# Performance work log

Hardware: AMD Instinct MI355X
Metric: run time of the kernel (lower is better)

Reference implementation:

```python
import jax, jax.numpy as jnp
import numpy as np

N = 25600   # total nodes
B = 256     # graphs / batch_size / LSTM seq length
F = 128     # num_feat
H = 256     # gnn_hidden
R = 512     # rnn_hidden == 2*H (forced by alm layer)
L = 2       # rnn_layers
V = 32000   # vocab
E = 409600  # edges
NPG = 100   # nodes per graph (forced by alm layer / attention reshape)


def setup_inputs() -> dict:
    key = jax.random.key(0)
    ks = jax.random.split(key, 20)
    def rn(k, shape, fan_in, scale=1.0):
        return jax.random.normal(k, shape, jnp.float32) * (scale / np.sqrt(fan_in))
    inp = {}
    inp['x'] = jax.random.normal(ks[0], (N, F), jnp.float32)
    inp['edge_index'] = jax.random.randint(ks[1], (2, E), 0, N)
    inp['bwd_edge_index'] = jnp.flip(inp['edge_index'], axis=0)
    inp['batch'] = jnp.arange(N) // NPG  # contiguous graphs, 100 nodes each
    inp['h0'] = jax.random.normal(ks[2], (L, 1, R), jnp.float32)
    inp['c0'] = jax.random.normal(ks[3], (L, 1, R), jnp.float32)
    inp['W_gnn'] = rn(ks[4], (F, H), F)
    inp['W_root'] = rn(ks[5], (H, H), H)
    inp['W_nbr'] = rn(ks[6], (H, H), H)
    inp['b_conv'] = jnp.zeros((H,), jnp.float32)
    D = 2 * H
    inp['W1'] = rn(ks[7], (D, D), D); inp['b1'] = jnp.zeros((D,), jnp.float32)
    inp['gamma'] = jnp.ones((D,), jnp.float32); inp['beta'] = jnp.zeros((D,), jnp.float32)
    inp['W2'] = rn(ks[8], (D, D), D); inp['b2'] = jnp.zeros((D,), jnp.float32)
    A = NPG * R + R  # alm input dim = rnn_hidden*100 + rnn_hidden
    inp['W_alm'] = rn(ks[9], (NPG, A), A, scale=0.1)
    inp['b_alm'] = jnp.ones((NPG,), jnp.float32)  # keeps alpha.sum() well away from 0
    inp['Wih0'] = rn(ks[10], (4 * R, D), D); inp['Whh0'] = rn(ks[11], (4 * R, R), R)
    inp['bih0'] = jnp.zeros((4 * R,), jnp.float32); inp['bhh0'] = jnp.zeros((4 * R,), jnp.float32)
    inp['Wih1'] = rn(ks[12], (4 * R, R), R); inp['Whh1'] = rn(ks[13], (4 * R, R), R)
    inp['bih1'] = jnp.zeros((4 * R,), jnp.float32); inp['bhh1'] = jnp.zeros((4 * R,), jnp.float32)
    inp['W_fc'] = rn(ks[14], (R, V), R); inp['b_fc'] = jnp.zeros((V,), jnp.float32)
    return inp


def _lstm_layer(inputs, h, c, Wih, Whh, bih, bhh):
    # inputs: (T, 1, in); carry h, c: (1, R). PyTorch gate order i, f, g, o.
    def step(carry, xt):
        h, c = carry
        g = xt @ Wih.T + bih + h @ Whh.T + bhh
        i, f, gg, o = jnp.split(g, 4, axis=-1)
        c = jax.nn.sigmoid(f) * c + jax.nn.sigmoid(i) * jnp.tanh(gg)
        h = jax.nn.sigmoid(o) * jnp.tanh(c)
        return (h, c), h
    (hT, cT), outs = jax.lax.scan(step, (h, c), inputs)
    return outs, hT, cT


def reference(x, edge_index, bwd_edge_index, batch, h0, c0, W_gnn, W_root, W_nbr, b_conv,
              W1, b1, gamma, beta, W2, b2, W_alm, b_alm,
              Wih0, Whh0, bih0, bhh0, Wih1, Whh1, bih1, bhh1, W_fc, b_fc):
    n = x.shape[0]
    x = x @ W_gnn  # (N, H)
    # GraphConv: out_i = W_root x_i + W_nbr * sum_{j->i} x_j + b.
    # (Original loops gnn_layers times from the SAME x, so only the last conv matters.)
    def conv(xx, ei):
        agg = jax.ops.segment_sum(xx[ei[0]], ei[1], num_segments=n)
        return xx @ W_root + agg @ W_nbr + b_conv
    fwd_x = jax.nn.relu(conv(x, edge_index))
    bwd_x = jax.nn.relu(conv(x, bwd_edge_index))
    xc = jnp.concatenate([fwd_x, bwd_x], axis=1)  # (N, 2H) == (N, R)
    # MLP [2H, 2H, 2H]: Lin -> BatchNorm(batch stats) -> ReLU -> (dropout off) -> Lin
    h1 = xc @ W1 + b1
    h1 = (h1 - h1.mean(0)) / jnp.sqrt(h1.var(0) + 1e-5) * gamma + beta
    x_mlp = jax.nn.relu(h1) @ W2 + b2
    # global mean pool over graphs
    counts = jax.ops.segment_sum(jnp.ones((n,), x_mlp.dtype), batch, num_segments=B)
    x_g = jax.ops.segment_sum(x_mlp, batch, num_segments=B) / counts[:, None]
    x_emb = x_g.reshape(B, 1, 2 * H)  # LSTM: seq_len=B, batch=1
    # attention over cell state (vectorized form of the nested loops):
    # alpha[l,b,:] = alm(cat(c0[l].flatten(), h3[b].flatten())); normalize by sum (NOT softmax);
    # new_c[l] = sum_b alpha[l,b,:] @ h3[b]
    h3 = xc.reshape(B, NPG, R)
    s = c0.reshape(L, R)
    Ws, Wh = W_alm[:, :R], W_alm[:, R:]
    alpha = (s @ Ws.T)[:, None, :] + (h3.reshape(B, NPG * R) @ Wh.T)[None] + b_alm  # (L,B,NPG)
    alpha = alpha / alpha.sum(-1, keepdims=True)
    new_c = jnp.einsum('lbk,bkd->ld', alpha, h3)  # (L, R)
    # 2-layer LSTM (eval mode: inter-layer dropout is identity)
    outs, hT0, cT0 = _lstm_layer(x_emb, h0[0], new_c[0:1], Wih0, Whh0, bih0, bhh0)
    outs, hT1, cT1 = _lstm_layer(outs, h0[1], new_c[1:2], Wih1, Whh1, bih1, bhh1)
    preds = (outs @ W_fc + b_fc)[:, -1, :]  # (B, V)
    return preds
```

## Files before the change

kernel.cpp:

```cpp
#include <hip/hip_runtime.h>
#include <math.h>

#define N_NODES 25600
#define F_IN    128
#define H_GNN   256
#define D_MLP   512
#define E_EDGE  409600
#define B_GR    256
#define NPG_    100
#define R_LSTM  512
#define V_OUT   32000

typedef __bf16 bf16x8 __attribute__((ext_vector_type(8)));
typedef float  f32x4  __attribute__((ext_vector_type(4)));
typedef unsigned short u16x8 __attribute__((ext_vector_type(8)));

__device__ __forceinline__ unsigned short f2bf(float x) {
    unsigned u = __builtin_bit_cast(unsigned, x);
    unsigned r = (u + 0x7FFFu + ((u >> 16) & 1u)) >> 16;
    return (unsigned short)r;
}

template<bool TRANSB>
__global__ __launch_bounds__(256)
void gemm_tile(const float* __restrict__ A, const float* __restrict__ B,
               float* __restrict__ C, const float* __restrict__ bias,
               int M, int N, int K, int lda, int ldb, int ldc, int kChunk)
{
    __shared__ float As[16][68];
    __shared__ float Bs[16][68];
    const int tid = threadIdx.x;
    const int n0 = blockIdx.x * 64;
    const int m0 = blockIdx.y * 64;
    const int z  = blockIdx.z;
    const int k0 = z * kChunk;
    const int k1 = min(K, k0 + kChunk);
    const int ty = tid >> 4, tx = tid & 15;
    float acc[4][4] = {};

    for (int kb = k0; kb < k1; kb += 16) {
        {
            const int r = tid >> 4, c = tid & 15;
            #pragma unroll
            for (int i = 0; i < 4; ++i) {
                int rr = r + i * 16;
                int gm = m0 + rr, gk = kb + c;
                As[c][rr] = (gm < M && gk < k1) ? A[gm * lda + gk] : 0.f;
            }
        }
        if (!TRANSB) {
            const int r = tid >> 6, c = tid & 63;
            #pragma unroll
            for (int i = 0; i < 4; ++i) {
                int rr = r + i * 4;
                int gk = kb + rr, gn = n0 + c;
                Bs[rr][c] = (gk < k1 && gn < N) ? B[gk * ldb + gn] : 0.f;
            }
        } else {
            const int r = tid & 15, c = tid >> 4;
            #pragma unroll
            for (int i = 0; i < 4; ++i) {
                int cc = c + i * 16;
                int gk = kb + r, gn = n0 + cc;
                Bs[r][cc] = (gk < k1 && gn < N) ? B[gn * ldb + gk] : 0.f;
            }
        }
        __syncthreads();
        #pragma unroll
        for (int kk = 0; kk < 16; ++kk) {
            float a[4], b[4];
            #pragma unroll
            for (int i = 0; i < 4; ++i) a[i] = As[kk][ty * 4 + i];
            #pragma unroll
            for (int j = 0; j < 4; ++j) b[j] = Bs[kk][tx * 4 + j];
            #pragma unroll
            for (int i = 0; i < 4; ++i)
                #pragma unroll
                for (int j = 0; j < 4; ++j)
                    acc[i][j] = fmaf(a[i], b[j], acc[i][j]);
        }
        __syncthreads();
    }

    const bool split = (gridDim.z > 1);
    #pragma unroll
    for (int i = 0; i < 4; ++i) {
        int gm = m0 + ty * 4 + i;
        if (gm >= M) continue;
        #pragma unroll
        for (int j = 0; j < 4; ++j) {
            int gn = n0 + tx * 4 + j;
            if (gn >= N) continue;
            float v = acc[i][j];
            if (bias != nullptr && z == 0) v += bias[gn];
            if (split) atomicAdd(&C[gm * ldc + gn], v);
            else       C[gm * ldc + gn] = v;
        }
    }
}

__global__ __launch_bounds__(256)
void gemm_f32_big(const float* __restrict__ A, const float* __restrict__ B,
                  float* __restrict__ C, const float* __restrict__ bias,
                  int M, int N, int K, int lda, int ldb, int ldc)
{
    __shared__ float As[8][128];
    __shared__ float Bs[8][128];
    const int tid = threadIdx.x;
    const int tx = tid & 15, ty = tid >> 4;
    const int n0 = blockIdx.x * 128, m0 = blockIdx.y * 128;
    float acc[8][8] = {};

    for (int kb = 0; kb < K; kb += 8) {
        {
            int r = tid >> 1, c = (tid & 1) * 4;
            float4 v = *(const float4*)(A + (long)(m0 + r) * lda + kb + c);
            As[c + 0][r] = v.x; As[c + 1][r] = v.y;
            As[c + 2][r] = v.z; As[c + 3][r] = v.w;
        }
        {
            int r = tid >> 5, c = (tid & 31) * 4;
            *(float4*)&Bs[r][c] = *(const float4*)(B + (long)(kb + r) * ldb + n0 + c);
        }
        __syncthreads();
        #pragma unroll
        for (int kk = 0; kk < 8; ++kk) {
            float a[8], b[8];
            *(float4*)&a[0] = *(const float4*)&As[kk][ty * 8];
            *(float4*)&a[4] = *(const float4*)&As[kk][ty * 8 + 4];
            *(float4*)&b[0] = *(const float4*)&Bs[kk][tx * 8];
            *(float4*)&b[4] = *(const float4*)&Bs[kk][tx * 8 + 4];
            #pragma unroll
            for (int i = 0; i < 8; ++i)
                #pragma unroll
                for (int j = 0; j < 8; ++j)
                    acc[i][j] = fmaf(a[i], b[j], acc[i][j]);
        }
        __syncthreads();
    }

    #pragma unroll
    for (int i = 0; i < 8; ++i) {
        int gm = m0 + ty * 8 + i;
        #pragma unroll
        for (int j = 0; j < 8; j += 4) {
            int gn = n0 + tx * 8 + j;
            float4 v = {acc[i][j], acc[i][j+1], acc[i][j+2], acc[i][j+3]};
            if (bias != nullptr) {
                v.x += bias[gn]; v.y += bias[gn + 1];
                v.z += bias[gn + 2]; v.w += bias[gn + 3];
            }
            *(float4*)(C + (long)gm * ldc + gn) = v;
        }
    }
}

__global__ __launch_bounds__(256)
void mfma_gemm(const unsigned short* __restrict__ A,
               const unsigned short* __restrict__ Bt,
               float* __restrict__ C, const float* __restrict__ bias,
               int M, int N, int K, int lda, int ldb, int ldc, int kChunk)
{
    __shared__ unsigned short As[128][40];
    __shared__ unsigned short Bs[128][40];
    const int tid  = threadIdx.x;
    const int lane = tid & 63;
    const int wv   = tid >> 6;
    const int wr   = wv >> 1, wc = wv & 1;
    const int n0 = blockIdx.x * 128;
    const int m0 = blockIdx.y * 128;
    const int z  = blockIdx.z;
    const int k0 = z * kChunk;
    const int k1 = min(K, k0 + kChunk);

    const int srow = tid >> 2;
    const int skoff = (tid & 3) * 8;

    f32x4 acc[4][4] = {};

    for (int kb = k0; kb < k1; kb += 32) {
        #pragma unroll
        for (int p = 0; p < 2; ++p) {
            int row = p * 64 + srow;
            u16x8 va = *(const u16x8*)(A + (long)(m0 + row) * lda + kb + skoff);
            *(u16x8*)&As[row][skoff] = va;
            int gb = n0 + row;
            u16x8 vb = {0, 0, 0, 0, 0, 0, 0, 0};
            if (gb < N) vb = *(const u16x8*)(Bt + (long)gb * ldb + kb + skoff);
            *(u16x8*)&Bs[row][skoff] = vb;
        }
        __syncthreads();
        bf16x8 af[4], bfr[4];
        #pragma unroll
        for (int fm = 0; fm < 4; ++fm)
            af[fm] = *(const bf16x8*)&As[wr * 64 + fm * 16 + (lane & 15)][(lane >> 4) * 8];
        #pragma unroll
        for (int fn = 0; fn < 4; ++fn)
            bfr[fn] = *(const bf16x8*)&Bs[wc * 64 + fn * 16 + (lane & 15)][(lane >> 4) * 8];
        #pragma unroll
        for (int fm = 0; fm < 4; ++fm)
            #pragma unroll
            for (int fn = 0; fn < 4; ++fn)
                acc[fm][fn] = __builtin_amdgcn_mfma_f32_16x16x32_bf16(
                    af[fm], bfr[fn], acc[fm][fn], 0, 0, 0);
        __syncthreads();
    }

    const bool split = (gridDim.z > 1);
    #pragma unroll
    for (int fm = 0; fm < 4; ++fm) {
        int row = m0 + wr * 64 + fm * 16 + ((lane >> 4) << 2);
        #pragma unroll
        for (int fn = 0; fn < 4; ++fn) {
            int col = n0 + wc * 64 + fn * 16 + (lane & 15);
            if (col >= N) continue;
            f32x4 v = acc[fm][fn];
            #pragma unroll
            for (int r = 0; r < 4; ++r) {
                float o = v[r];
                if (bias != nullptr && z == 0) o += bias[col];
                if (split) atomicAdd(&C[(long)(row + r) * ldc + col], o);
                else       C[(long)(row + r) * ldc + col] = o;
            }
        }
    }
}

__global__ void castbf(const float* __restrict__ in, unsigned short* __restrict__ out,
                       long n) {
    long stride = (long)gridDim.x * blockDim.x * 4;
    for (long j = ((long)blockIdx.x * blockDim.x + threadIdx.x) * 4; j < n; j += stride) {
        float4 v = *(const float4*)(in + j);
        ushort4 o;
        o.x = f2bf(v.x); o.y = f2bf(v.y); o.z = f2bf(v.z); o.w = f2bf(v.w);
        *(ushort4*)(out + j) = o;
    }
}
__global__ void cast_strided(const float* __restrict__ in, unsigned short* __restrict__ out,
                             int cols, long ldin, long off) {
    const int r = blockIdx.y;
    int c = (blockIdx.x * blockDim.x + threadIdx.x) * 4;
    if (c < cols) {
        float4 v = *(const float4*)(in + (long)r * ldin + off + c);
        ushort4 o;
        o.x = f2bf(v.x); o.y = f2bf(v.y); o.z = f2bf(v.z); o.w = f2bf(v.w);
        *(ushort4*)(out + (long)r * cols + c) = o;
    }
}
__global__ __launch_bounds__(256)
void transcast(const float* __restrict__ in, unsigned short* __restrict__ out,
               int R, int C) {
    __shared__ unsigned short t[64][72];
    const int c0 = blockIdx.x * 64, r0 = blockIdx.y * 64;
    const int tid = threadIdx.x;
    const int rr = tid >> 2, cg = (tid & 3) * 16;
    #pragma unroll
    for (int i = 0; i < 4; ++i) {
        float4 v = *(const float4*)(in + (long)(r0 + rr) * C + c0 + cg + i * 4);
        t[cg + i * 4 + 0][rr] = f2bf(v.x);
        t[cg + i * 4 + 1][rr] = f2bf(v.y);
        t[cg + i * 4 + 2][rr] = f2bf(v.z);
        t[cg + i * 4 + 3][rr] = f2bf(v.w);
    }
    __syncthreads();
    const int cc = tid >> 2, kg = (tid & 3) * 16;
    #pragma unroll
    for (int i = 0; i < 2; ++i) {
        u16x8 v = *(const u16x8*)&t[cc][kg + i * 8];
        *(u16x8*)(out + (long)(c0 + cc) * R + r0 + kg + i * 8) = v;
    }
}

__global__ void zero_f32(float* p, long n) {
    for (long i = (long)blockIdx.x * blockDim.x + threadIdx.x; i < n;
         i += (long)gridDim.x * blockDim.x) p[i] = 0.f;
}
__global__ void zero_i32(int* p, long n) {
    for (long i = (long)blockIdx.x * blockDim.x + threadIdx.x; i < n;
         i += (long)gridDim.x * blockDim.x) p[i] = 0;
}
__global__ void addvec_kernel(const float* a, const float* b, float* o, int n) {
    int i = blockIdx.x * blockDim.x + threadIdx.x;
    if (i < n) o[i] = a[i] + b[i];
}
__global__ void concat_bias(const float* __restrict__ b_conv, float* bc2) {
    int i = blockIdx.x * blockDim.x + threadIdx.x;
    if (i < 512) bc2[i] = (i < 256) ? b_conv[i] : 0.f;
}

__global__ void hist_kernel(const int* __restrict__ key, int* counts, int E) {
    int i = blockIdx.x * blockDim.x + threadIdx.x;
    if (i < E) atomicAdd(&counts[key[i]], 1);
}
__global__ __launch_bounds__(256)
void scan_chunk(const int* __restrict__ counts, int* __restrict__ rowptr,
                int* __restrict__ tops, int n) {
    __shared__ int buf[256];
    const int tid = threadIdx.x;
    int i = blockIdx.x * 256 + tid;
    int v = (i < n) ? counts[i] : 0;
    buf[tid] = v;
    __syncthreads();
    for (int off = 1; off < 256; off <<= 1) {
        int add = (tid >= off) ? buf[tid - off] : 0;
        __syncthreads();
        buf[tid] += add;
        __syncthreads();
    }
    if (i < n) rowptr[i + 1] = buf[tid];
    if (tid == 255) tops[blockIdx.x] = buf[255];
}
__global__ __launch_bounds__(128)
void scan_tops(int* tops, int nt) {
    __shared__ int b[128];
    int tid = threadIdx.x;
    int v = (tid < nt) ? tops[tid] : 0;
    b[tid] = v;
    __syncthreads();
    for (int off = 1; off < 128; off <<= 1) {
        int add = (tid >= off) ? b[tid - off] : 0;
        __syncthreads();
        b[tid] += add;
        __syncthreads();
    }
    if (tid < nt) tops[tid] = b[tid] - v;
}
__global__ void scan_fixup(const int* __restrict__ counts, int* __restrict__ rowptr,
                           int* __restrict__ cursor, const int* __restrict__ tops, int n) {
    int i = blockIdx.x * blockDim.x + threadIdx.x;
    if (i < n) {
        int r = rowptr[i + 1] + tops[i >> 8];
        rowptr[i + 1] = r;
        cursor[i] = r - counts[i];
        if (i == 0) rowptr[0] = 0;
    }
}
__global__ void scatter_kernel(const int* __restrict__ key, const int* __restrict__ val,
                               int* cursor, int* sorted, int E) {
    int i = blockIdx.x * blockDim.x + threadIdx.x;
    if (i < E) {
        int pos = atomicAdd(&cursor[key[i]], 1);
        sorted[pos] = val[i];
    }
}
__global__ __launch_bounds__(256)
void agg_conv_kernel(const float* __restrict__ xrn,
                     const int* __restrict__ rowptr, const int* __restrict__ sorted,
                     float* __restrict__ xc, int outOff) {
    const int n = blockIdx.x, tid = threadIdx.x;
    float acc = xrn[(long)n * 512 + tid];
    const int s = rowptr[n], e = rowptr[n + 1];
    for (int t = s; t < e; ++t)
        acc += xrn[(long)sorted[t] * 512 + 256 + tid];
    xc[(long)n * 512 + outOff + tid] = fmaxf(acc, 0.f);
}

__global__ __launch_bounds__(512)
void colstat_kernel(const float* __restrict__ h1, float* colsum, float* colsq) {
    const int c = threadIdx.x;
    const int r0 = blockIdx.x * 128;
    float s = 0.f, s2 = 0.f;
    for (int r = 0; r < 128; ++r) {
        float v = h1[(long)(r0 + r) * D_MLP + c];
        s += v; s2 += v * v;
    }
    atomicAdd(&colsum[c], s);
    atomicAdd(&colsq[c], s2);
}
__global__ void finalize_stats(const float* colsum, const float* colsq,
                               const float* gamma, const float* beta,
                               float* scalev, float* shiftv) {
    int c = threadIdx.x;
    float m  = colsum[c] * (1.f / N_NODES);
    float vr = colsq[c] * (1.f / N_NODES) - m * m;
    float g  = gamma[c] * rsqrtf(vr + 1e-5f);
    scalev[c] = g;
    shiftv[c] = beta[c] - m * g;
}
__global__ void norm_relu(float* h, const float* __restrict__ sc,
                          const float* __restrict__ sh, long n) {
    for (long i = (long)blockIdx.x * blockDim.x + threadIdx.x; i < n;
         i += (long)gridDim.x * blockDim.x) {
        int c = (int)(i & 511);
        h[i] = fmaxf(fmaf(h[i], sc[c], sh[c]), 0.f);
    }
}
__global__ __launch_bounds__(512)
void pool_kernel(const float* __restrict__ hrelu, float* P) {
    const int b = blockIdx.x, c = threadIdx.x;
    float s = 0.f;
    for (int i = 0; i < NPG_; ++i) s += hrelu[(long)(b * NPG_ + i) * D_MLP + c];
    P[b * D_MLP + c] = s * (1.f / NPG_);
}
__global__ void sw_kernel(const float* __restrict__ c0, const float* __restrict__ W_alm,
                          float* sW) {
    int i = blockIdx.x * blockDim.x + threadIdx.x;
    if (i < 2 * NPG_) {
        int l = i / NPG_, p = i % NPG_;
        float s = 0.f;
        for (int k = 0; k < R_LSTM; ++k) s += c0[l * R_LSTM + k] * W_alm[p * 51712 + k];
        sW[l * NPG_ + p] = s;
    }
}
__global__ __launch_bounds__(128)
void alpha_kernel(const float* __restrict__ sW, const float* __restrict__ hW,
                  const float* __restrict__ b_alm, float* __restrict__ alpha) {
    const int lb = blockIdx.x;
    const int l = lb >> 8, b = lb & 255;
    const int p = threadIdx.x;
    __shared__ float red[128];
    float v = 0.f;
    if (p < NPG_) v = sW[l * NPG_ + p] + hW[b * NPG_ + p] + b_alm[p];
    red[p] = v;
    __syncthreads();
    for (int s = 64; s > 0; s >>= 1) {
        if (p < s) red[p] += red[p + s];
        __syncthreads();
    }
    float inv = 1.f / red[0];
    if (p < NPG_) alpha[lb * NPG_ + p] = v * inv;
}
__global__ __launch_bounds__(512)
void newc_kernel(const float* __restrict__ alpha, const float* __restrict__ xc,
                 float* new_c) {
    const int l = blockIdx.y, chunk = blockIdx.x, c = threadIdx.x;
    const int r0 = chunk * 800;
    float acc = 0.f;
    for (int r = r0; r < r0 + 800; ++r)
        acc += alpha[l * N_NODES + r] * xc[(long)r * D_MLP + c];
    atomicAdd(&new_c[l * D_MLP + c], acc);
}

#define CANARY 0x7FC00000u
#define SPIN_MAX 20000

__device__ __forceinline__ unsigned coh_load_u(const unsigned* p) {
    return __hip_atomic_load(p, __ATOMIC_RELAXED, __HIP_MEMORY_SCOPE_AGENT);
}
__device__ __forceinline__ void coh_store_f(float* p, float v) {
    __hip_atomic_store(p, v, __ATOMIC_RELAXED, __HIP_MEMORY_SCOPE_AGENT);
}

__global__ void lstm_init_kernel(const float* __restrict__ h0,
                                 float* h0buf, float* h1buf) {
    int i = blockIdx.x * blockDim.x + threadIdx.x;
    if (i < 512) { h0buf[i] = h0[i]; h1buf[i] = h0[512 + i]; }
    for (int j = 512 + i; j < 257 * 512; j += gridDim.x * blockDim.x) {
        ((unsigned*)h0buf)[j] = CANARY;
        ((unsigned*)h1buf)[j] = CANARY;
    }
}

__global__ __launch_bounds__(512)
void lstm_kernel(const float* __restrict__ inp0, const float* __restrict__ Whh0,
                 const float* __restrict__ Wih1, const float* __restrict__ Whh1,
                 const float* __restrict__ b1s, const float* __restrict__ new_c,
                 float* h0buf, float* h1buf)
{
    const int tid  = threadIdx.x;
    const int lane = tid & 63;
    const int w    = tid >> 6;
    const int blk  = blockIdx.x;
    const int layer = blk >> 5;
    const int base  = (blk & 31) * 16;
    const int gate  = lane >> 4;
    const int hid   = lane & 15;
    const int rowg  = gate * 512 + base + hid;

    __shared__ float partial[2][8][64];

    if (layer == 0) {
        float wr[64];
        {
            const float4* wp = (const float4*)(Whh0 + (long)rowg * 512 + w * 64);
            #pragma unroll
            for (int i = 0; i < 16; ++i) {
                float4 v = wp[i];
                wr[4*i] = v.x; wr[4*i+1] = v.y; wr[4*i+2] = v.z; wr[4*i+3] = v.w;
            }
        }
        float c = (w == 0 && lane < 16) ? new_c[base + lane] : 0.f;
        const unsigned* src_u = (const unsigned*)h0buf + w * 64 + lane;
        for (int t = 0; t < 256; ++t) {
            float ipv = (w == 0) ? inp0[t * 2048 + rowg] : 0.f;
            unsigned hu; int guard = 0;
            for (;;) {
                hu = coh_load_u(src_u + t * 512);
                if (!__any(hu == CANARY)) break;
                if (++guard > SPIN_MAX) break;
                if (guard > 32) __builtin_amdgcn_s_sleep(1);
            }
            float hv = __uint_as_float(hu);
            float acc = 0.f;
            #pragma unroll
            for (int j = 0; j < 64; ++j)
                acc = fmaf(wr[j], __shfl(hv, j), acc);
            partial[t & 1][w][lane] = acc;
            __syncthreads();
            if (w == 0) {
                float g = ipv;
                #pragma unroll
                for (int ww = 0; ww < 8; ++ww) g += partial[t & 1][ww][lane];
                float a = (gate == 2) ? tanhf(g) : 1.f / (1.f + expf(-g));
                float fv = __shfl(a, lane + 16);
                float gv = __shfl(a, lane + 32);
                float ov = __shfl(a, lane + 48);
                if (lane < 16) {
                    c = fv * c + a * gv;
                    float h = ov * tanhf(c);
                    coh_store_f(h0buf + (t + 1) * 512 + base + lane, h);
                }
            }
        }
    } else {
        const float* Wsel = (w < 4) ? Wih1 : Whh1;
        const int koff = (w & 3) * 128;
        float wrA[64], wrB[64];
        {
            const float4* wp = (const float4*)(Wsel + (long)rowg * 512 + koff);
            #pragma unroll
            for (int i = 0; i < 16; ++i) {
                float4 v = wp[i];
                wrA[4*i] = v.x; wrA[4*i+1] = v.y; wrA[4*i+2] = v.z; wrA[4*i+3] = v.w;
            }
            #pragma unroll
            for (int i = 0; i < 16; ++i) {
                float4 v = wp[16 + i];
                wrB[4*i] = v.x; wrB[4*i+1] = v.y; wrB[4*i+2] = v.z; wrB[4*i+3] = v.w;
            }
        }
        float bsum = (w == 0) ? b1s[rowg] : 0.f;
        float c = (w == 0 && lane < 16) ? new_c[512 + base + lane] : 0.f;
        for (int t = 0; t < 256; ++t) {
            const unsigned* xsrc = (w < 4)
                ? (const unsigned*)h0buf + (t + 1) * 512 + koff
                : (const unsigned*)h1buf + t * 512 + koff;
            unsigned hu0, hu1; int guard = 0;
            for (;;) {
                hu0 = coh_load_u(xsrc + lane);
                hu1 = coh_load_u(xsrc + 64 + lane);
                if (!__any((hu0 == CANARY) || (hu1 == CANARY))) break;
                if (++guard > SPIN_MAX) break;
                if (guard > 32) __builtin_amdgcn_s_sleep(1);
            }
            float hv0 = __uint_as_float(hu0), hv1 = __uint_as_float(hu1);
            float acc = 0.f;
            #pragma unroll
            for (int j = 0; j < 64; ++j)
                acc = fmaf(wrA[j], __shfl(hv0, j), acc);
            #pragma unroll
            for (int j = 0; j < 64; ++j)
                acc = fmaf(wrB[j], __shfl(hv1, j), acc);
            partial[t & 1][w][lane] = acc;
            __syncthreads();
            if (w == 0) {
                float g = bsum;
                #pragma unroll
                for (int ww = 0; ww < 8; ++ww) g += partial[t & 1][ww][lane];
                float a = (gate == 2) ? tanhf(g) : 1.f / (1.f + expf(-g));
                float fv = __shfl(a, lane + 16);
                float gv = __shfl(a, lane + 32);
                float ov = __shfl(a, lane + 48);
                if (lane < 16) {
                    c = fv * c + a * gv;
                    float h = ov * tanhf(c);
                    coh_store_f(h1buf + (t + 1) * 512 + base + lane, h);
                }
            }
        }
    }
}

extern "C" void kernel_launch(void* const* d_in, const int* in_sizes, int n_in,
                              void* d_out, int out_size, void* d_ws, size_t ws_size,
                              hipStream_t stream)
{
    const float* x      = (const float*)d_in[0];
    const int*   ei     = (const int*)d_in[1];
    const float* h0     = (const float*)d_in[4];
    const float* c0     = (const float*)d_in[5];
    const float* W_gnn  = (const float*)d_in[6];
    const float* W_root = (const float*)d_in[7];
    const float* W_nbr  = (const float*)d_in[8];
    const float* b_conv = (const float*)d_in[9];
    const float* W1     = (const float*)d_in[10];
    const float* b1     = (const float*)d_in[11];
    const float* gamma  = (const float*)d_in[12];
    const float* beta   = (const float*)d_in[13];
    const float* W2     = (const float*)d_in[14];
    const float* b2     = (const float*)d_in[15];
    const float* W_alm  = (const float*)d_in[16];
    const float* b_alm  = (const float*)d_in[17];
    const float* Wih0   = (const float*)d_in[18];
    const float* Whh0   = (const float*)d_in[19];
    const float* bih0   = (const float*)d_in[20];
    const float* bhh0   = (const float*)d_in[21];
    const float* Wih1   = (const float*)d_in[22];
    const float* Whh1   = (const float*)d_in[23];
    const float* bih1   = (const float*)d_in[24];
    const float* bhh1   = (const float*)d_in[25];
    const float* W_fc   = (const float*)d_in[26];
    const float* b_fc   = (const float*)d_in[27];
    float* out = (float*)d_out;
    float* ws  = (float*)d_ws;

    const int* ei0 = ei;
    const int* ei1 = ei + E_EDGE;

    float* xrn = ws;
    float* h1m = ws;
    unsigned short* Wfct  = (unsigned short*)ws;
    unsigned short* Walmb = (unsigned short*)(ws + 8500000L);
    unsigned short* ob    = (unsigned short*)(ws + 11200000L);
    float* xc = ws + 13107200L;
    long o = 26214400L;
    float* Wc    = ws + o; o += 65536;
    int*   counts= (int*)(ws + o); o += 25600;
    int*   rowptr= (int*)(ws + o); o += 25601;
    int*   cursor= (int*)(ws + o); o += 25600;
    int*   sorted= (int*)(ws + o); o += 409600;
    int*   tops  = (int*)(ws + o); o += 128;
    float* colsum= ws + o; o += 512;
    float* colsq = ws + o; o += 512;
    float* scalev= ws + o; o += 512;
    float* shiftv= ws + o; o += 512;
    float* P     = ws + o; o += 131072;
    float* x_g   = ws + o; o += 131072;
    float* hW    = ws + o; o += 25600;
    float* sW    = ws + o; o += 200;
    float* alphav= ws + o; o += 51200;
    float* newc  = ws + o; o += 1024;
    float* b0s   = ws + o; o += 2048;
    float* b1s   = ws + o; o += 2048;
    float* bc2   = ws + o; o += 512;
    unsigned short* xcb = (unsigned short*)(ws + o);
    float* inp0  = ws + o;
    float* h0st  = ws + o + 524288;
    float* h1st  = ws + o + 655872;
    o += 6553600;

    gemm_tile<false><<<dim3(4, 2, 1), 256, 0, stream>>>(W_gnn, W_root, Wc, nullptr,
        128, 256, 256, 256, 256, 512, 256);
    gemm_tile<false><<<dim3(4, 2, 1), 256, 0, stream>>>(W_gnn, W_nbr, Wc + 256, nullptr,
        128, 256, 256, 256, 256, 512, 256);
    concat_bias<<<dim3(2), 256, 0, stream>>>(b_conv, bc2);
    gemm_f32_big<<<dim3(4, 200), 256, 0, stream>>>(x, Wc, xrn, bc2,
        N_NODES, 512, 128, 128, 512, 512);
    zero_i32<<<dim3(100), 256, 0, stream>>>(counts, 25600);
    hist_kernel<<<dim3(1600), 256, 0, stream>>>(ei1, counts, E_EDGE);
    scan_chunk<<<dim3(100), 256, 0, stream>>>(counts, rowptr, tops, 25600);
    scan_tops<<<dim3(1), 128, 0, stream>>>(tops, 100);
    scan_fixup<<<dim3(100), 256, 0, stream>>>(counts, rowptr, cursor, tops, 25600);
    scatter_kernel<<<dim3(1600), 256, 0, stream>>>(ei1, ei0, cursor, sorted, E_EDGE);
    agg_conv_kernel<<<dim3(25600), 256, 0, stream>>>(xrn, rowptr, sorted, xc, 0);
    zero_i32<<<dim3(100), 256, 0, stream>>>(counts, 25600);
    hist_kernel<<<dim3(1600), 256, 0, stream>>>(ei0, counts, E_EDGE);
    scan_chunk<<<dim3(100), 256, 0, stream>>>(counts, rowptr, tops, 25600);
    scan_tops<<<dim3(1), 128, 0, stream>>>(tops, 100);
    scan_fixup<<<dim3(100), 256, 0, stream>>>(counts, rowptr, cursor, tops, 25600);
    scatter_kernel<<<dim3(1600), 256, 0, stream>>>(ei0, ei1, cursor, sorted, E_EDGE);
    agg_conv_kernel<<<dim3(25600), 256, 0, stream>>>(xrn, rowptr, sorted, xc, 256);
    gemm_f32_big<<<dim3(4, 200), 256, 0, stream>>>(xc, W1, h1m, b1,
        N_NODES, 512, 512, 512, 512, 512);
    zero_f32<<<dim3(4), 256, 0, stream>>>(colsum, 1024);
    colstat_kernel<<<dim3(200), 512, 0, stream>>>(h1m, colsum, colsq);
    finalize_stats<<<dim3(1), 512, 0, stream>>>(colsum, colsq, gamma, beta, scalev, shiftv);
    norm_relu<<<dim3(2048), 256, 0, stream>>>(h1m, scalev, shiftv, (long)N_NODES * 512);
    pool_kernel<<<dim3(256), 512, 0, stream>>>(h1m, P);
    gemm_tile<false><<<dim3(8, 4, 1), 256, 0, stream>>>(P, W2, x_g, b2,
        256, 512, 512, 512, 512, 512, 512);
    transcast<<<dim3(500, 8), 256, 0, stream>>>(W_fc, Wfct, 512, V_OUT);
    cast_strided<<<dim3(50, 100), 256, 0, stream>>>(W_alm, Walmb, 51200, 51712L, 512L);
    castbf<<<dim3(1024), 256, 0, stream>>>(xc, xcb, 13107200L);
    zero_f32<<<dim3(25), 256, 0, stream>>>(hW, 25600);
    mfma_gemm<<<dim3(1, 2, 32), 256, 0, stream>>>(xcb, Walmb, hW, nullptr,
        256, 100, 51200, 51200, 51200, 100, 1600);
    sw_kernel<<<dim3(1), 256, 0, stream>>>(c0, W_alm, sW);
    alpha_kernel<<<dim3(512), 128, 0, stream>>>(sW, hW, b_alm, alphav);
    zero_f32<<<dim3(1), 256, 0, stream>>>(newc, 1024);
    newc_kernel<<<dim3(32, 2), 512, 0, stream>>>(alphav, xc, newc);
    addvec_kernel<<<dim3(8), 256, 0, stream>>>(bih0, bhh0, b0s, 2048);
    addvec_kernel<<<dim3(8), 256, 0, stream>>>(bih1, bhh1, b1s, 2048);
    gemm_tile<true><<<dim3(32, 4, 1), 256, 0, stream>>>(x_g, Wih0, inp0, b0s,
        256, 2048, 512, 512, 512, 2048, 512);
    lstm_init_kernel<<<dim3(64), 512, 0, stream>>>(h0, h0st, h1st);
    lstm_kernel<<<dim3(64), 512, 0, stream>>>(inp0, Whh0, Wih1, Whh1, b1s, newc,
                                              h0st, h1st);
    castbf<<<dim3(128), 256, 0, stream>>>(h1st + 512, ob, 131072L);
    mfma_gemm<<<dim3(250, 2, 1), 256, 0, stream>>>(ob, Wfct, out, b_fc,
        256, V_OUT, 512, 512, 512, V_OUT, 512);
}
```

Baseline: 1.868 ms.

## Restructure LSTM recurrence to split-K LDS dot products and fuse small kernels

The persistent LSTM kernel now stages h into shared memory once per step and has each 8-lane group compute one gate row via split-K with xor-shuffle reduction. This replaces the 64 cross-lane shuffles per step and the single-wave gate finalization, and every wave now finishes its own two hidden units. Separately, norm+relu is fused into the pooling kernel, removing a full read/write pass over the 25600x512 activation. The tiny bias/sW kernels are merged into one prep kernel to cut launches. The risk is higher register use in layer 1 (128 weights per thread), which could cause spilling.

```diff
diff --git a/kernel.cpp b/kernel.cpp
--- a/kernel.cpp
+++ b/kernel.cpp
@@ -279,13 +279,29 @@
     for (long i = (long)blockIdx.x * blockDim.x + threadIdx.x; i < n;
          i += (long)gridDim.x * blockDim.x) p[i] = 0;
 }
-__global__ void addvec_kernel(const float* a, const float* b, float* o, int n) {
-    int i = blockIdx.x * blockDim.x + threadIdx.x;
-    if (i < n) o[i] = a[i] + b[i];
-}
-__global__ void concat_bias(const float* __restrict__ b_conv, float* bc2) {
-    int i = blockIdx.x * blockDim.x + threadIdx.x;
-    if (i < 512) bc2[i] = (i < 256) ? b_conv[i] : 0.f;
+__global__ __launch_bounds__(256)
+void prep_kernel(const float* __restrict__ bih0, const float* __restrict__ bhh0,
+                 const float* __restrict__ bih1, const float* __restrict__ bhh1,
+                 const float* __restrict__ b_conv, const float* __restrict__ c0,
+                 const float* __restrict__ W_alm,
+                 float* b0s, float* b1s, float* bc2, float* sW) {
+    const int b = blockIdx.x, t = threadIdx.x;
+    if (b < 8) {
+        int i = b * 256 + t;
+        b0s[i] = bih0[i] + bhh0[i];
+        b1s[i] = bih1[i] + bhh1[i];
+    } else if (b == 8) {
+        bc2[t] = b_conv[t];
+        bc2[t + 256] = 0.f;
+    } else {
+        if (t < 2 * NPG_) {
+            int l = t / NPG_, p = t % NPG_;
+            float s = 0.f;
+            for (int k = 0; k < R_LSTM; ++k)
+                s += c0[l * R_LSTM + k] * W_alm[(long)p * 51712 + k];
+            sW[l * NPG_ + p] = s;
+        }
+    }
 }
 
 __global__ void hist_kernel(const int* __restrict__ key, int* counts, int E) {
@@ -377,30 +393,17 @@
     scalev[c] = g;
     shiftv[c] = beta[c] - m * g;
 }
-__global__ void norm_relu(float* h, const float* __restrict__ sc,
-                          const float* __restrict__ sh, long n) {
-    for (long i = (long)blockIdx.x * blockDim.x + threadIdx.x; i < n;
-         i += (long)gridDim.x * blockDim.x) {
-        int c = (int)(i & 511);
-        h[i] = fmaxf(fmaf(h[i], sc[c], sh[c]), 0.f);
-    }
-}
 __global__ __launch_bounds__(512)
-void pool_kernel(const float* __restrict__ hrelu, float* P) {
+void fused_norm_pool(const float* __restrict__ h1, const float* __restrict__ sc,
+                     const float* __restrict__ sh, float* __restrict__ P) {
     const int b = blockIdx.x, c = threadIdx.x;
+    const float scv = sc[c], shv = sh[c];
     float s = 0.f;
-    for (int i = 0; i < NPG_; ++i) s += hrelu[(long)(b * NPG_ + i) * D_MLP + c];
+    for (int i = 0; i < NPG_; ++i) {
+        float v = h1[(long)(b * NPG_ + i) * D_MLP + c];
+        s += fmaxf(fmaf(v, scv, shv), 0.f);
+    }
     P[b * D_MLP + c] = s * (1.f / NPG_);
-}
-__global__ void sw_kernel(const float* __restrict__ c0, const float* __restrict__ W_alm,
-                          float* sW) {
-    int i = blockIdx.x * blockDim.x + threadIdx.x;
-    if (i < 2 * NPG_) {
-        int l = i / NPG_, p = i % NPG_;
-        float s = 0.f;
-        for (int k = 0; k < R_LSTM; ++k) s += c0[l * R_LSTM + k] * W_alm[p * 51712 + k];
-        sW[l * NPG_ + p] = s;
-    }
 }
 __global__ __launch_bounds__(128)
 void alpha_kernel(const float* __restrict__ sW, const float* __restrict__ hW,
@@ -463,109 +466,116 @@
     const int blk  = blockIdx.x;
     const int layer = blk >> 5;
     const int base  = (blk & 31) * 16;
-    const int gate  = lane >> 4;
-    const int hid   = lane & 15;
-    const int rowg  = gate * 512 + base + hid;
-
-    __shared__ float partial[2][8][64];
+    const int r8   = lane >> 3;
+    const int s    = lane & 7;
+    const int gate = r8 >> 1;
+    const int q    = r8 & 1;
+    const int row  = gate * 512 + base + w * 2 + q;
+    const int ql   = lane & 1;
+
+    __shared__ float hbs[2][8][132];
 
     if (layer == 0) {
         float wr[64];
         {
-            const float4* wp = (const float4*)(Whh0 + (long)rowg * 512 + w * 64);
+            const float4* wp = (const float4*)(Whh0 + (long)row * 512 + s * 64);
             #pragma unroll
             for (int i = 0; i < 16; ++i) {
                 float4 v = wp[i];
                 wr[4*i] = v.x; wr[4*i+1] = v.y; wr[4*i+2] = v.z; wr[4*i+3] = v.w;
             }
         }
-        float c = (w == 0 && lane < 16) ? new_c[base + lane] : 0.f;
-        const unsigned* src_u = (const unsigned*)h0buf + w * 64 + lane;
+        float c = (lane < 2) ? new_c[base + w * 2 + lane] : 0.f;
+        const unsigned* src = (const unsigned*)h0buf + w * 64 + lane;
         for (int t = 0; t < 256; ++t) {
-            float ipv = (w == 0) ? inp0[t * 2048 + rowg] : 0.f;
+            float ipv = inp0[t * 2048 + row];
             unsigned hu; int guard = 0;
             for (;;) {
-                hu = coh_load_u(src_u + t * 512);
+                hu = coh_load_u(src + (long)t * 512);
                 if (!__any(hu == CANARY)) break;
                 if (++guard > SPIN_MAX) break;
                 if (guard > 32) __builtin_amdgcn_s_sleep(1);
             }
-            float hv = __uint_as_float(hu);
+            const int p = t & 1;
+            hbs[p][w][lane] = __uint_as_float(hu);
+            __syncthreads();
             float acc = 0.f;
-            #pragma unroll
-            for (int j = 0; j < 64; ++j)
-                acc = fmaf(wr[j], __shfl(hv, j), acc);
-            partial[t & 1][w][lane] = acc;
-            __syncthreads();
-            if (w == 0) {
-                float g = ipv;
-                #pragma unroll
-                for (int ww = 0; ww < 8; ++ww) g += partial[t & 1][ww][lane];
-                float a = (gate == 2) ? tanhf(g) : 1.f / (1.f + expf(-g));
-                float fv = __shfl(a, lane + 16);
-                float gv = __shfl(a, lane + 32);
-                float ov = __shfl(a, lane + 48);
-                if (lane < 16) {
-                    c = fv * c + a * gv;
-                    float h = ov * tanhf(c);
-                    coh_store_f(h0buf + (t + 1) * 512 + base + lane, h);
-                }
+            const f32x4* hrow = (const f32x4*)&hbs[p][s][0];
+            #pragma unroll
+            for (int jj = 0; jj < 16; ++jj) {
+                f32x4 hv = hrow[jj];
+                acc = fmaf(wr[4*jj + 0], hv.x, acc);
+                acc = fmaf(wr[4*jj + 1], hv.y, acc);
+                acc = fmaf(wr[4*jj + 2], hv.z, acc);
+                acc = fmaf(wr[4*jj + 3], hv.w, acc);
+            }
+            acc += __shfl_xor(acc, 1);
+            acc += __shfl_xor(acc, 2);
+            acc += __shfl_xor(acc, 4);
+            float g = acc + ipv;
+            float a = (gate == 2) ? tanhf(g) : 1.f / (1.f + expf(-g));
+            float ai = __shfl(a,      ql * 8);
+            float af = __shfl(a, 16 + ql * 8);
+            float ag = __shfl(a, 32 + ql * 8);
+            float ao = __shfl(a, 48 + ql * 8);
+            if (lane < 2) {
+                c = af * c + ai * ag;
+                float h = ao * tanhf(c);
+                coh_store_f(h0buf + (long)(t + 1) * 512 + base + w * 2 + lane, h);
             }
         }
     } else {
-        const float* Wsel = (w < 4) ? Wih1 : Whh1;
-        const int koff = (w & 3) * 128;
-        float wrA[64], wrB[64];
+        float wr[128];
         {
-            const float4* wp = (const float4*)(Wsel + (long)rowg * 512 + koff);
-            #pragma unroll
-            for (int i = 0; i < 16; ++i) {
+            const float* Wsel = (s < 4) ? Wih1 : Whh1;
+            const float4* wp = (const float4*)(Wsel + (long)row * 512 + (s & 3) * 128);
+            #pragma unroll
+            for (int i = 0; i < 32; ++i) {
                 float4 v = wp[i];
-                wrA[4*i] = v.x; wrA[4*i+1] = v.y; wrA[4*i+2] = v.z; wrA[4*i+3] = v.w;
-            }
-            #pragma unroll
-            for (int i = 0; i < 16; ++i) {
-                float4 v = wp[16 + i];
-                wrB[4*i] = v.x; wrB[4*i+1] = v.y; wrB[4*i+2] = v.z; wrB[4*i+3] = v.w;
-            }
-        }
-        float bsum = (w == 0) ? b1s[rowg] : 0.f;
-        float c = (w == 0 && lane < 16) ? new_c[512 + base + lane] : 0.f;
+                wr[4*i] = v.x; wr[4*i+1] = v.y; wr[4*i+2] = v.z; wr[4*i+3] = v.w;
+            }
+        }
+        const float bsum = b1s[row];
+        float c = (lane < 2) ? new_c[512 + base + w * 2 + lane] : 0.f;
+        const int slot = w >> 1, jof = (w & 1) * 64;
         for (int t = 0; t < 256; ++t) {
-            const unsigned* xsrc = (w < 4)
-                ? (const unsigned*)h0buf + (t + 1) * 512 + koff
-                : (const unsigned*)h1buf + t * 512 + koff;
+            const unsigned* s0 = (const unsigned*)h0buf + (long)(t + 1) * 512 + w * 64 + lane;
+            const unsigned* s1 = (const unsigned*)h1buf + (long)t * 512 + w * 64 + lane;
             unsigned hu0, hu1; int guard = 0;
             for (;;) {
-                hu0 = coh_load_u(xsrc + lane);
-                hu1 = coh_load_u(xsrc + 64 + lane);
+                hu0 = coh_load_u(s0);
+                hu1 = coh_load_u(s1);
                 if (!__any((hu0 == CANARY) || (hu1 == CANARY))) break;
                 if (++guard > SPIN_MAX) break;
                 if (guard > 32) __builtin_amdgcn_s_sleep(1);
             }
-            float hv0 = __uint_as_float(hu0), hv1 = __uint_as_float(hu1);
+            const int p = t & 1;
+            hbs[p][slot][jof + lane]     = __uint_as_float(hu0);
+            hbs[p][4 + slot][jof + lane] = __uint_as_float(hu1);
+            __syncthreads();
             float acc = 0.f;
-            #pragma unroll
-            for (int j = 0; j < 64; ++j)
-                acc = fmaf(wrA[j], __shfl(hv0, j), acc);
-            #pragma unroll
-            for (int j = 0; j < 64; ++j)
-                acc = fmaf(wrB[j], __shfl(hv1, j), acc);
-            partial[t & 1][w][lane] = acc;
-            __syncthreads();
-            if (w == 0) {
-                float g = bsum;
-                #pragma unroll
-                for (int ww = 0; ww < 8; ++ww) g += partial[t & 1][ww][lane];
-                float a = (gate == 2) ? tanhf(g) : 1.f / (1.f + expf(-g));
-                float fv = __shfl(a, lane + 16);
-                float gv = __shfl(a, lane + 32);
-                float ov = __shfl(a, lane + 48);
-                if (lane < 16) {
-                    c = fv * c + a * gv;
-                    float h = ov * tanhf(c);
-                    coh_store_f(h1buf + (t + 1) * 512 + base + lane, h);
-                }
+            const f32x4* hrow = (const f32x4*)&hbs[p][s][0];
+            #pragma unroll
+            for (int jj = 0; jj < 32; ++jj) {
+                f32x4 hv = hrow[jj];
+                acc = fmaf(wr[4*jj + 0], hv.x, acc);
+                acc = fmaf(wr[4*jj + 1], hv.y, acc);
+                acc = fmaf(wr[4*jj + 2], hv.z, acc);
+                acc = fmaf(wr[4*jj + 3], hv.w, acc);
+            }
+            acc += __shfl_xor(acc, 1);
+            acc += __shfl_xor(acc, 2);
+            acc += __shfl_xor(acc, 4);
+            float g = acc + bsum;
+            float a = (gate == 2) ? tanhf(g) : 1.f / (1.f + expf(-g));
+            float ai = __shfl(a,      ql * 8);
+            float af = __shfl(a, 16 + ql * 8);
+            float ag = __shfl(a, 32 + ql * 8);
+            float ao = __shfl(a, 48 + ql * 8);
+            if (lane < 2) {
+                c = af * c + ai * ag;
+                float h = ao * tanhf(c);
+                coh_store_f(h1buf + (long)(t + 1) * 512 + base + w * 2 + lane, h);
             }
         }
     }
@@ -639,11 +649,12 @@
     float* h1st  = ws + o + 655872;
     o += 6553600;
 
+    prep_kernel<<<dim3(10), 256, 0, stream>>>(bih0, bhh0, bih1, bhh1, b_conv, c0,
+                                              W_alm, b0s, b1s, bc2, sW);
     gemm_tile<false><<<dim3(4, 2, 1), 256, 0, stream>>>(W_gnn, W_root, Wc, nullptr,
         128, 256, 256, 256, 256, 512, 256);
     gemm_tile<false><<<dim3(4, 2, 1), 256, 0, stream>>>(W_gnn, W_nbr, Wc + 256, nullptr,
         128, 256, 256, 256, 256, 512, 256);
-    concat_bias<<<dim3(2), 256, 0, stream>>>(b_conv, bc2);
     gemm_f32_big<<<dim3(4, 200), 256, 0, stream>>>(x, Wc, xrn, bc2,
         N_NODES, 512, 128, 128, 512, 512);
     zero_i32<<<dim3(100), 256, 0, stream>>>(counts, 25600);
@@ -665,8 +676,7 @@
     zero_f32<<<dim3(4), 256, 0, stream>>>(colsum, 1024);
     colstat_kernel<<<dim3(200), 512, 0, stream>>>(h1m, colsum, colsq);
     finalize_stats<<<dim3(1), 512, 0, stream>>>(colsum, colsq, gamma, beta, scalev, shiftv);
-    norm_relu<<<dim3(2048), 256, 0, stream>>>(h1m, scalev, shiftv, (long)N_NODES * 512);
-    pool_kernel<<<dim3(256), 512, 0, stream>>>(h1m, P);
+    fused_norm_pool<<<dim3(256), 512, 0, stream>>>(h1m, scalev, shiftv, P);
     gemm_tile<false><<<dim3(8, 4, 1), 256, 0, stream>>>(P, W2, x_g, b2,
         256, 512, 512, 512, 512, 512, 512);
     transcast<<<dim3(500, 8), 256, 0, stream>>>(W_fc, Wfct, 512, V_OUT);
@@ -675,12 +685,9 @@
     zero_f32<<<dim3(25), 256, 0, stream>>>(hW, 25600);
     mfma_gemm<<<dim3(1, 2, 32), 256, 0, stream>>>(xcb, Walmb, hW, nullptr,
         256, 100, 51200, 51200, 51200, 100, 1600);
-    sw_kernel<<<dim3(1), 256, 0, stream>>>(c0, W_alm, sW);
     alpha_kernel<<<dim3(512), 128, 0, stream>>>(sW, hW, b_alm, alphav);
     zero_f32<<<dim3(1), 256, 0, stream>>>(newc, 1024);
     newc_kernel<<<dim3(32, 2), 512, 0, stream>>>(alphav, xc, newc);
-    addvec_kernel<<<dim3(8), 256, 0, stream>>>(bih0, bhh0, b0s, 2048);
-    addvec_kernel<<<dim3(8), 256, 0, stream>>>(bih1, bhh1, b1s, 2048);
     gemm_tile<true><<<dim3(32, 4, 1), 256, 0, stream>>>(x_g, Wih0, inp0, b0s,
         256, 2048, 512, 512, 512, 2048, 512);
     lstm_init_kernel<<<dim3(64), 512, 0, stream>>>(h0, h0st, h1st);
```

Result: slower. 1.930 ms (+3.3%).

## Fuse output projection into persistent LSTM kernel and merge small prep kernels

Applied to the files above, without the earlier changes.

Extra persistent blocks are added to the LSTM kernel. Each holds a 128-column slice of W_fc in registers, spins on each new layer-1 hidden state, and writes the prediction row as soon as that step finishes. This removes the W_fc transpose-cast, the bf16 cast of the outputs and the final MFMA GEMM, overlapping the vocab projection with the serial recurrence. The projection now runs in fp32 FMAs instead of bf16 MFMA. The bias-add, bias-concat and sW kernels are merged into one prep kernel, and norm+relu is fused into pooling so the full h1 write-back is avoided. It assumes all 314 blocks are co-resident for the spin-waits, and the 128-float register arrays raise register pressure.

```diff
diff --git a/kernel.cpp b/kernel.cpp
--- a/kernel.cpp
+++ b/kernel.cpp
@@ -247,29 +247,6 @@
         *(ushort4*)(out + (long)r * cols + c) = o;
     }
 }
-__global__ __launch_bounds__(256)
-void transcast(const float* __restrict__ in, unsigned short* __restrict__ out,
-               int R, int C) {
-    __shared__ unsigned short t[64][72];
-    const int c0 = blockIdx.x * 64, r0 = blockIdx.y * 64;
-    const int tid = threadIdx.x;
-    const int rr = tid >> 2, cg = (tid & 3) * 16;
-    #pragma unroll
-    for (int i = 0; i < 4; ++i) {
-        float4 v = *(const float4*)(in + (long)(r0 + rr) * C + c0 + cg + i * 4);
-        t[cg + i * 4 + 0][rr] = f2bf(v.x);
-        t[cg + i * 4 + 1][rr] = f2bf(v.y);
-        t[cg + i * 4 + 2][rr] = f2bf(v.z);
-        t[cg + i * 4 + 3][rr] = f2bf(v.w);
-    }
-    __syncthreads();
-    const int cc = tid >> 2, kg = (tid & 3) * 16;
-    #pragma unroll
-    for (int i = 0; i < 2; ++i) {
-        u16x8 v = *(const u16x8*)&t[cc][kg + i * 8];
-        *(u16x8*)(out + (long)(c0 + cc) * R + r0 + kg + i * 8) = v;
-    }
-}
 
 __global__ void zero_f32(float* p, long n) {
     for (long i = (long)blockIdx.x * blockDim.x + threadIdx.x; i < n;
@@ -279,13 +256,29 @@
     for (long i = (long)blockIdx.x * blockDim.x + threadIdx.x; i < n;
          i += (long)gridDim.x * blockDim.x) p[i] = 0;
 }
-__global__ void addvec_kernel(const float* a, const float* b, float* o, int n) {
-    int i = blockIdx.x * blockDim.x + threadIdx.x;
-    if (i < n) o[i] = a[i] + b[i];
-}
-__global__ void concat_bias(const float* __restrict__ b_conv, float* bc2) {
-    int i = blockIdx.x * blockDim.x + threadIdx.x;
-    if (i < 512) bc2[i] = (i < 256) ? b_conv[i] : 0.f;
+__global__ __launch_bounds__(256)
+void prep_kernel(const float* __restrict__ bih0, const float* __restrict__ bhh0,
+                 const float* __restrict__ bih1, const float* __restrict__ bhh1,
+                 const float* __restrict__ b_conv, const float* __restrict__ c0,
+                 const float* __restrict__ W_alm,
+                 float* b0s, float* b1s, float* bc2, float* sW) {
+    const int b = blockIdx.x, t = threadIdx.x;
+    if (b < 8) {
+        int i = b * 256 + t;
+        b0s[i] = bih0[i] + bhh0[i];
+        b1s[i] = bih1[i] + bhh1[i];
+    } else if (b == 8) {
+        bc2[t] = b_conv[t];
+        bc2[t + 256] = 0.f;
+    } else {
+        if (t < 2 * NPG_) {
+            int l = t / NPG_, p = t % NPG_;
+            float s = 0.f;
+            for (int k = 0; k < R_LSTM; ++k)
+                s += c0[l * R_LSTM + k] * W_alm[(long)p * 51712 + k];
+            sW[l * NPG_ + p] = s;
+        }
+    }
 }
 
 __global__ void hist_kernel(const int* __restrict__ key, int* counts, int E) {
@@ -377,30 +370,17 @@
     scalev[c] = g;
     shiftv[c] = beta[c] - m * g;
 }
-__global__ void norm_relu(float* h, const float* __restrict__ sc,
-                          const float* __restrict__ sh, long n) {
-    for (long i = (long)blockIdx.x * blockDim.x + threadIdx.x; i < n;
-         i += (long)gridDim.x * blockDim.x) {
-        int c = (int)(i & 511);
-        h[i] = fmaxf(fmaf(h[i], sc[c], sh[c]), 0.f);
-    }
-}
 __global__ __launch_bounds__(512)
-void pool_kernel(const float* __restrict__ hrelu, float* P) {
+void fused_norm_pool(const float* __restrict__ h1, const float* __restrict__ sc,
+                     const float* __restrict__ sh, float* __restrict__ P) {
     const int b = blockIdx.x, c = threadIdx.x;
+    const float scv = sc[c], shv = sh[c];
     float s = 0.f;
-    for (int i = 0; i < NPG_; ++i) s += hrelu[(long)(b * NPG_ + i) * D_MLP + c];
+    for (int i = 0; i < NPG_; ++i) {
+        float v = h1[(long)(b * NPG_ + i) * D_MLP + c];
+        s += fmaxf(fmaf(v, scv, shv), 0.f);
+    }
     P[b * D_MLP + c] = s * (1.f / NPG_);
-}
-__global__ void sw_kernel(const float* __restrict__ c0, const float* __restrict__ W_alm,
-                          float* sW) {
-    int i = blockIdx.x * blockDim.x + threadIdx.x;
-    if (i < 2 * NPG_) {
-        int l = i / NPG_, p = i % NPG_;
-        float s = 0.f;
-        for (int k = 0; k < R_LSTM; ++k) s += c0[l * R_LSTM + k] * W_alm[p * 51712 + k];
-        sW[l * NPG_ + p] = s;
-    }
 }
 __global__ __launch_bounds__(128)
 void alpha_kernel(const float* __restrict__ sW, const float* __restrict__ hW,
@@ -455,21 +435,24 @@
 void lstm_kernel(const float* __restrict__ inp0, const float* __restrict__ Whh0,
                  const float* __restrict__ Wih1, const float* __restrict__ Whh1,
                  const float* __restrict__ b1s, const float* __restrict__ new_c,
-                 float* h0buf, float* h1buf)
+                 float* h0buf, float* h1buf,
+                 const float* __restrict__ W_fc, const float* __restrict__ b_fc,
+                 float* __restrict__ out)
 {
     const int tid  = threadIdx.x;
     const int lane = tid & 63;
     const int w    = tid >> 6;
     const int blk  = blockIdx.x;
-    const int layer = blk >> 5;
-    const int base  = (blk & 31) * 16;
-    const int gate  = lane >> 4;
-    const int hid   = lane & 15;
-    const int rowg  = gate * 512 + base + hid;
 
     __shared__ float partial[2][8][64];
-
-    if (layer == 0) {
+    __shared__ float hlds[512];
+    __shared__ float pred_part[4][128];
+
+    if (blk < 32) {
+        const int base  = blk * 16;
+        const int gate  = lane >> 4;
+        const int hid   = lane & 15;
+        const int rowg  = gate * 512 + base + hid;
         float wr[64];
         {
             const float4* wp = (const float4*)(Whh0 + (long)rowg * 512 + w * 64);
@@ -480,12 +463,12 @@
             }
         }
         float c = (w == 0 && lane < 16) ? new_c[base + lane] : 0.f;
-        const unsigned* src_u = (const unsigned*)h0buf + w * 64 + lane;
+        const unsigned* src = (const unsigned*)h0buf + w * 64 + lane;
         for (int t = 0; t < 256; ++t) {
             float ipv = (w == 0) ? inp0[t * 2048 + rowg] : 0.f;
             unsigned hu; int guard = 0;
             for (;;) {
-                hu = coh_load_u(src_u + t * 512);
+                hu = coh_load_u(src + (long)t * 512);
                 if (!__any(hu == CANARY)) break;
                 if (++guard > SPIN_MAX) break;
                 if (guard > 32) __builtin_amdgcn_s_sleep(1);
@@ -508,11 +491,15 @@
                 if (lane < 16) {
                     c = fv * c + a * gv;
                     float h = ov * tanhf(c);
-                    coh_store_f(h0buf + (t + 1) * 512 + base + lane, h);
+                    coh_store_f(h0buf + (long)(t + 1) * 512 + base + lane, h);
                 }
             }
         }
-    } else {
+    } else if (blk < 64) {
+        const int base  = (blk - 32) * 16;
+        const int gate  = lane >> 4;
+        const int hid   = lane & 15;
+        const int rowg  = gate * 512 + base + hid;
         const float* Wsel = (w < 4) ? Wih1 : Whh1;
         const int koff = (w & 3) * 128;
         float wrA[64], wrB[64];
@@ -533,8 +520,8 @@
         float c = (w == 0 && lane < 16) ? new_c[512 + base + lane] : 0.f;
         for (int t = 0; t < 256; ++t) {
             const unsigned* xsrc = (w < 4)
-                ? (const unsigned*)h0buf + (t + 1) * 512 + koff
-                : (const unsigned*)h1buf + t * 512 + koff;
+                ? (const unsigned*)h0buf + (long)(t + 1) * 512 + koff
+                : (const unsigned*)h1buf + (long)t * 512 + koff;
             unsigned hu0, hu1; int guard = 0;
             for (;;) {
                 hu0 = coh_load_u(xsrc + lane);
@@ -564,8 +551,55 @@
                 if (lane < 16) {
                     c = fv * c + a * gv;
                     float h = ov * tanhf(c);
-                    coh_store_f(h1buf + (t + 1) * 512 + base + lane, h);
+                    coh_store_f(h1buf + (long)(t + 1) * 512 + base + lane, h);
                 }
+            }
+        }
+    } else {
+        const int pb  = blk - 64;
+        const int c0  = pb * 128;
+        const int col = tid & 127;
+        const int q   = tid >> 7;
+        float wr[128];
+        #pragma unroll 16
+        for (int j = 0; j < 128; ++j)
+            wr[j] = W_fc[(long)(q * 128 + j) * V_OUT + c0 + col];
+        const float bv = b_fc[c0 + col];
+        for (int t = 0; t < 256; ++t) {
+            if (w == 0) {
+                const unsigned* src = (const unsigned*)h1buf + (long)(t + 1) * 512 + lane * 8;
+                unsigned v[8]; int guard = 0;
+                for (;;) {
+                    bool bad = false;
+                    #pragma unroll
+                    for (int i = 0; i < 8; ++i) {
+                        v[i] = coh_load_u(src + i);
+                        bad = bad || (v[i] == CANARY);
+                    }
+                    if (!__any(bad)) break;
+                    if (++guard > SPIN_MAX) break;
+                    if (guard > 32) __builtin_amdgcn_s_sleep(1);
+                }
+                #pragma unroll
+                for (int i = 0; i < 8; ++i) hlds[lane * 8 + i] = __uint_as_float(v[i]);
+            }
+            __syncthreads();
+            float acc = 0.f;
+            const f32x4* hp = (const f32x4*)&hlds[q * 128];
+            #pragma unroll
+            for (int j4 = 0; j4 < 32; ++j4) {
+                f32x4 hv = hp[j4];
+                acc = fmaf(wr[4*j4 + 0], hv.x, acc);
+                acc = fmaf(wr[4*j4 + 1], hv.y, acc);
+                acc = fmaf(wr[4*j4 + 2], hv.z, acc);
+                acc = fmaf(wr[4*j4 + 3], hv.w, acc);
+            }
+            pred_part[q][col] = acc;
+            __syncthreads();
+            if (tid < 128) {
+                float s = pred_part[0][tid] + pred_part[1][tid]
+                        + pred_part[2][tid] + pred_part[3][tid] + bv;
+                out[(long)t * V_OUT + c0 + tid] = s;
             }
         }
     }
@@ -609,9 +643,7 @@
 
     float* xrn = ws;
     float* h1m = ws;
-    unsigned short* Wfct  = (unsigned short*)ws;
     unsigned short* Walmb = (unsigned short*)(ws + 8500000L);
-    unsigned short* ob    = (unsigned short*)(ws + 11200000L);
     float* xc = ws + 13107200L;
     long o = 26214400L;
     float* Wc    = ws + o; o += 65536;
@@ -639,11 +671,12 @@
     float* h1st  = ws + o + 655872;
     o += 6553600;
 
+    prep_kernel<<<dim3(10), 256, 0, stream>>>(bih0, bhh0, bih1, bhh1, b_conv, c0,
+                                              W_alm, b0s, b1s, bc2, sW);
     gemm_tile<false><<<dim3(4, 2, 1), 256, 0, stream>>>(W_gnn, W_root, Wc, nullptr,
         128, 256, 256, 256, 256, 512, 256);
     gemm_tile<false><<<dim3(4, 2, 1), 256, 0, stream>>>(W_gnn, W_nbr, Wc + 256, nullptr,
         128, 256, 256, 256, 256, 512, 256);
-    concat_bias<<<dim3(2), 256, 0, stream>>>(b_conv, bc2);
     gemm_f32_big<<<dim3(4, 200), 256, 0, stream>>>(x, Wc, xrn, bc2,
         N_NODES, 512, 128, 128, 512, 512);
     zero_i32<<<dim3(100), 256, 0, stream>>>(counts, 25600);
@@ -665,28 +698,20 @@
     zero_f32<<<dim3(4), 256, 0, stream>>>(colsum, 1024);
     colstat_kernel<<<dim3(200), 512, 0, stream>>>(h1m, colsum, colsq);
     finalize_stats<<<dim3(1), 512, 0, stream>>>(colsum, colsq, gamma, beta, scalev, shiftv);
-    norm_relu<<<dim3(2048), 256, 0, stream>>>(h1m, scalev, shiftv, (long)N_NODES * 512);
-    pool_kernel<<<dim3(256), 512, 0, stream>>>(h1m, P);
+    fused_norm_pool<<<dim3(256), 512, 0, stream>>>(h1m, scalev, shiftv, P);
     gemm_tile<false><<<dim3(8, 4, 1), 256, 0, stream>>>(P, W2, x_g, b2,
         256, 512, 512, 512, 512, 512, 512);
-    transcast<<<dim3(500, 8), 256, 0, stream>>>(W_fc, Wfct, 512, V_OUT);
     cast_strided<<<dim3(50, 100), 256, 0, stream>>>(W_alm, Walmb, 51200, 51712L, 512L);
     castbf<<<dim3(1024), 256, 0, stream>>>(xc, xcb, 13107200L);
     zero_f32<<<dim3(25), 256, 0, stream>>>(hW, 25600);
     mfma_gemm<<<dim3(1, 2, 32), 256, 0, stream>>>(xcb, Walmb, hW, nullptr,
         256, 100, 51200, 51200, 51200, 100, 1600);
-    sw_kernel<<<dim3(1), 256, 0, stream>>>(c0, W_alm, sW);
     alpha_kernel<<<dim3(512), 128, 0, stream>>>(sW, hW, b_alm, alphav);
     zero_f32<<<dim3(1), 256, 0, stream>>>(newc, 1024);
     newc_kernel<<<dim3(32, 2), 512, 0, stream>>>(alphav, xc, newc);
-    addvec_kernel<<<dim3(8), 256, 0, stream>>>(bih0, bhh0, b0s, 2048);
-    addvec_kernel<<<dim3(8), 256, 0, stream>>>(bih1, bhh1, b1s, 2048);
     gemm_tile<true><<<dim3(32, 4, 1), 256, 0, stream>>>(x_g, Wih0, inp0, b0s,
         256, 2048, 512, 512, 512, 2048, 512);
     lstm_init_kernel<<<dim3(64), 512, 0, stream>>>(h0, h0st, h1st);
-    lstm_kernel<<<dim3(64), 512, 0, stream>>>(inp0, Whh0, Wih1, Whh1, b1s, newc,
-                                              h0st, h1st);
-    castbf<<<dim3(128), 256, 0, stream>>>(h1st + 512, ob, 131072L);
-    mfma_gemm<<<dim3(250, 2, 1), 256, 0, stream>>>(ob, Wfct, out, b_fc,
-        256, V_OUT, 512, 512, 512, V_OUT, 512);
-}
+    lstm_kernel<<<dim3(314), 512, 0, stream>>>(inp0, Whh0, Wih1, Whh1, b1s, newc,
+                                               h0st, h1st, W_fc, b_fc, out);
+}
```

Result: slower. 4.430 ms (+137.1%).
